# Optimization experiments

Hardware: AMD Instinct MI355X
Metric: run time of the kernel (lower is better)

Reference implementation:

```python
import jax, jax.numpy as jnp
import numpy as np

EMBED = 1024

def setup_inputs() -> dict:
    key = jax.random.key(0)
    ks = jax.random.split(key, 10)
    B, S, E = 4, 2048, EMBED
    inv = 1.0 / np.sqrt(E)
    return {
        "query": jax.random.normal(ks[0], (B, S, E), jnp.float32),
        "key": jax.random.normal(ks[1], (B, S, E), jnp.float32),
        "value": jax.random.normal(ks[2], (B, S, E), jnp.float32),
        "attn_mask": jnp.zeros((B, S, S), jnp.float32),
        "Wq": jax.random.normal(ks[3], (E, E), jnp.float32) * inv,
        "bq": jnp.zeros((E,), jnp.float32),
        "Wk": jax.random.normal(ks[4], (E, E), jnp.float32) * inv,
        "bk": jnp.zeros((E,), jnp.float32),
        "Wv": jax.random.normal(ks[5], (E, E), jnp.float32) * inv,
        "bv": jnp.zeros((E,), jnp.float32),
    }

def reference(query, key, value, attn_mask, Wq, bq, Wk, bk, Wv, bv):
    E = query.shape[-1]
    q = query @ Wq.T + bq            # [B,S,E]
    k = key @ Wk.T + bk              # [B,S,E]
    v = value @ Wv.T + bv            # [B,S,E]
    scores = jnp.einsum('bse,bte->bst', q, k) / jnp.sqrt(jnp.float32(E))
    scores = scores + attn_mask      # [B,S,S]
    attn = jax.nn.softmax(scores, axis=-1)
    return jnp.einsum('bst,bte->bse', attn, v)
```

## Files before the change

### kernel.cpp

```cpp
#include <hip/hip_runtime.h>
#include <cstdint>
#include <cstddef>

typedef __bf16 bf16;
typedef __bf16 bf16x8 __attribute__((ext_vector_type(8)));
typedef float  f32x4  __attribute__((ext_vector_type(4)));

#define NB 4
#define SS 2048
#define EE 1024

#define BUFB   24576
#define LDS3   (3 * BUFB)
#define BUFB64 49152
#define LDS64  (3 * BUFB64)

static __device__ __forceinline__ void glds16(const bf16* g, void* l)
{
    __builtin_amdgcn_global_load_lds(
        (const __attribute__((address_space(1))) unsigned int*)g,
        (__attribute__((address_space(3))) unsigned int*)l,
        16, 0, 0);
}

static __device__ __forceinline__ void swz_block(int& bx, int& by, int& bz)
{
    const int nx = gridDim.x, ny = gridDim.y;
    const int nwg = nx * ny * gridDim.z;
    int lin = blockIdx.x + nx * (blockIdx.y + ny * blockIdx.z);
    const int per = nwg >> 3;
    lin = (lin & 7) * per + (lin >> 3);
    bz = lin / (nx * ny);
    const int r = lin - bz * nx * ny;
    by = r / nx;
    bx = r - by * nx;
}

static __device__ __forceinline__ void kloop32(
    const bf16* __restrict__ A, const bf16* __restrict__ Bm,
    int lda, int ldb, int nt, char* lds, int m0, int n0, int tid,
    f32x4 acc[4][4])
{
    constexpr int NBUF = 3;
    const int lane = tid & 63, w = tid >> 6;
    const int wm = w >> 2, wn = w & 3;
    const int lr = lane & 15, kq = lane >> 4;
    const int cb = ((kq ^ ((lr >> 1) & 3)) << 4);

    const int srow   = tid >> 2;
    const int chunkL = (tid & 3) ^ ((srow >> 1) & 3);
    const bf16* Asrc = A  + (size_t)(m0 + srow) * lda + chunkL * 8;
    const bf16* Bsrc = Bm + (size_t)(n0 + srow) * ldb + chunkL * 8;
    const int wofs = w << 10;

#pragma unroll
    for (int p = 0; p < NBUF - 1; ++p) {
        char* d = lds + p * BUFB + wofs;
        const int kt = p * 32;
        glds16(Asrc + kt,                     d);
        glds16(Bsrc + kt,                     d + 8192);
        glds16(Bsrc + (size_t)128 * ldb + kt, d + 16384);
    }
    asm volatile("s_waitcnt vmcnt(3)" ::: "memory");
    __builtin_amdgcn_sched_barrier(0);
    __builtin_amdgcn_s_barrier();
    __builtin_amdgcn_sched_barrier(0);

    int rb = 0, sb = NBUF - 1;
    for (int t = 0; t < nt; ++t) {
        char* la = lds + rb * BUFB;
        char* lb = la + 8192;
        const int ts = (t + NBUF - 1 < nt) ? t + NBUF - 1 : nt - 1;
        const int kt = ts * 32;
        char* d = lds + sb * BUFB + wofs;

        bf16x8 af[4], bg[4];
#pragma unroll
        for (int m = 0; m < 4; ++m)
            af[m] = *(const bf16x8*)(la + (wm * 64 + m * 16 + lr) * 64 + cb);
#pragma unroll
        for (int n = 0; n < 4; ++n)
            bg[n] = *(const bf16x8*)(lb + (wn * 64 + n * 16 + lr) * 64 + cb);

        glds16(Asrc + kt,                     d);
        glds16(Bsrc + kt,                     d + 8192);
        glds16(Bsrc + (size_t)128 * ldb + kt, d + 16384);

        __builtin_amdgcn_s_setprio(1);
#pragma unroll
        for (int m = 0; m < 4; ++m)
#pragma unroll
            for (int n = 0; n < 4; ++n)
                acc[m][n] = __builtin_amdgcn_mfma_f32_16x16x32_bf16(af[m], bg[n], acc[m][n], 0, 0, 0);
        __builtin_amdgcn_s_setprio(0);

        if (t < nt - 1) {
            asm volatile("s_waitcnt vmcnt(3)" ::: "memory");
            __builtin_amdgcn_sched_barrier(0);
            __builtin_amdgcn_s_barrier();
            __builtin_amdgcn_sched_barrier(0);
        }
        rb = (rb + 1 == NBUF) ? 0 : rb + 1;
        sb = (sb + 1 == NBUF) ? 0 : sb + 1;
    }
    asm volatile("s_waitcnt vmcnt(0)" ::: "memory");
}

static __device__ __forceinline__ void kloop32w(
    const bf16* __restrict__ A, const bf16* __restrict__ Bm,
    int lda, int ldb, int nt, char* lds, int m0, int n0, int tid,
    f32x4 acc[4][8])
{
    constexpr int NBUF = 3;
    const int lane = tid & 63, w = tid >> 6;
    const int wm = w >> 1, wn = w & 1;
    const int lr = lane & 15, kq = lane >> 4;
    const int cb = ((kq ^ ((lr >> 1) & 3)) << 4);

    const int srow   = tid >> 2;
    const int chunkL = (tid & 3) ^ ((srow >> 1) & 3);
    const bf16* Asrc = A  + (size_t)(m0 + srow) * lda + chunkL * 8;
    const bf16* Bsrc = Bm + (size_t)(n0 + srow) * ldb + chunkL * 8;
    const int wofs = w << 10;

#pragma unroll
    for (int p = 0; p < NBUF - 1; ++p) {
        char* d = lds + p * BUFB + wofs;
        const int kt = p * 32;
        glds16(Asrc + kt,                      d);
        glds16(Asrc + (size_t)64  * lda + kt,  d + 4096);
        glds16(Bsrc + kt,                      d + 8192);
        glds16(Bsrc + (size_t)64  * ldb + kt,  d + 12288);
        glds16(Bsrc + (size_t)128 * ldb + kt,  d + 16384);
        glds16(Bsrc + (size_t)192 * ldb + kt,  d + 20480);
    }
    asm volatile("s_waitcnt vmcnt(6)" ::: "memory");
    __builtin_amdgcn_sched_barrier(0);
    __builtin_amdgcn_s_barrier();
    __builtin_amdgcn_sched_barrier(0);

    int rb = 0, sb = NBUF - 1;
    for (int t = 0; t < nt; ++t) {
        char* la = lds + rb * BUFB;
        char* lb = la + 8192;
        const int ts = (t + NBUF - 1 < nt) ? t + NBUF - 1 : nt - 1;
        const int kt = ts * 32;
        char* d = lds + sb * BUFB + wofs;

        bf16x8 af[4], bg[8];
#pragma unroll
        for (int m = 0; m < 4; ++m)
            af[m] = *(const bf16x8*)(la + (wm * 64 + m * 16 + lr) * 64 + cb);
#pragma unroll
        for (int n = 0; n < 8; ++n)
            bg[n] = *(const bf16x8*)(lb + (wn * 128 + n * 16 + lr) * 64 + cb);

        glds16(Asrc + kt,                      d);
        glds16(Asrc + (size_t)64  * lda + kt,  d + 4096);
        glds16(Bsrc + kt,                      d + 8192);
        glds16(Bsrc + (size_t)64  * ldb + kt,  d + 12288);
        glds16(Bsrc + (size_t)128 * ldb + kt,  d + 16384);
        glds16(Bsrc + (size_t)192 * ldb + kt,  d + 20480);

        __builtin_amdgcn_s_setprio(1);
#pragma unroll
        for (int m = 0; m < 4; ++m)
#pragma unroll
            for (int n = 0; n < 8; ++n)
                acc[m][n] = __builtin_amdgcn_mfma_f32_16x16x32_bf16(af[m], bg[n], acc[m][n], 0, 0, 0);
        __builtin_amdgcn_s_setprio(0);

        if (t < nt - 1) {
            asm volatile("s_waitcnt vmcnt(6)" ::: "memory");
            __builtin_amdgcn_sched_barrier(0);
            __builtin_amdgcn_s_barrier();
            __builtin_amdgcn_sched_barrier(0);
        }
        rb = (rb + 1 == NBUF) ? 0 : rb + 1;
        sb = (sb + 1 == NBUF) ? 0 : sb + 1;
    }
    asm volatile("s_waitcnt vmcnt(0)" ::: "memory");
}

static __device__ __forceinline__ void kloop64(
    const bf16* __restrict__ A, const bf16* __restrict__ Bm,
    int lda, int ldb, int nt, char* lds, int m0, int n0, int tid,
    f32x4 acc[4][4])
{
    const int lane = tid & 63, w = tid >> 6;
    const int wm = w >> 2, wn = w & 3;
    const int lr = lane & 15, kq = lane >> 4;
    const int axor = (lr & 7) << 4;

    const int srow   = tid >> 3;
    const int chunkL = (tid & 7) ^ (srow & 7);
    const bf16* Asrc = A  + (size_t)(m0 + srow) * lda + chunkL * 8;
    const bf16* Bsrc = Bm + (size_t)(n0 + srow) * ldb + chunkL * 8;
    const int wofs = w << 10;

#pragma unroll
    for (int p = 0; p < 2; ++p) {
        char* d = lds + p * BUFB64 + wofs;
        const int kt = p * 64;
        glds16(Asrc + kt,                        d);
        glds16(Asrc + (size_t)64 * lda + kt,     d + 8192);
        glds16(Bsrc + kt,                        d + 16384);
        glds16(Bsrc + (size_t)64 * ldb + kt,     d + 16384 + 8192);
        glds16(Bsrc + (size_t)128 * ldb + kt,    d + 16384 + 16384);
        glds16(Bsrc + (size_t)192 * ldb + kt,    d + 16384 + 24576);
    }
    asm volatile("s_waitcnt vmcnt(6)" ::: "memory");
    __builtin_amdgcn_sched_barrier(0);
    __builtin_amdgcn_s_barrier();
    __builtin_amdgcn_sched_barrier(0);

    for (int t = 0; t < nt; ++t) {
        char* la = lds + (t % 3) * BUFB64;
        char* lb = la + 16384;
        char* sa = lds + ((t + 2) % 3) * BUFB64;
        const bool st = (t + 2) < nt;
        const int kt = (t + 2) * 64;

        bf16x8 af[4], bg[4];
        {
            const int cbk = (kq * 16) ^ axor;
#pragma unroll
            for (int m = 0; m < 4; ++m)
                af[m] = *(const bf16x8*)(la + (wm * 64 + m * 16 + lr) * 128 + cbk);
#pragma unroll
            for (int n = 0; n < 4; ++n)
                bg[n] = *(const bf16x8*)(lb + (wn * 64 + n * 16 + lr) * 128 + cbk);
            if (st) {
                glds16(Asrc + kt,                    sa + wofs);
                glds16(Asrc + (size_t)64 * lda + kt, sa + 8192 + wofs);
                glds16(Bsrc + kt,                    sa + 16384 + wofs);
            }
            __builtin_amdgcn_s_setprio(1);
#pragma unroll
            for (int m = 0; m < 4; ++m)
#pragma unroll
                for (int n = 0; n < 4; ++n)
                    acc[m][n] = __builtin_amdgcn_mfma_f32_16x16x32_bf16(af[m], bg[n], acc[m][n], 0, 0, 0);
            __builtin_amdgcn_s_setprio(0);
        }
        {
            const int cbk = (64 + kq * 16) ^ axor;
#pragma unroll
            for (int m = 0; m < 4; ++m)
                af[m] = *(const bf16x8*)(la + (wm * 64 + m * 16 + lr) * 128 + cbk);
#pragma unroll
            for (int n = 0; n < 4; ++n)
                bg[n] = *(const bf16x8*)(lb + (wn * 64 + n * 16 + lr) * 128 + cbk);
            if (st) {
                glds16(Bsrc + (size_t)64 * ldb + kt,  sa + 16384 + 8192 + wofs);
                glds16(Bsrc + (size_t)128 * ldb + kt, sa + 16384 + 16384 + wofs);
                glds16(Bsrc + (size_t)192 * ldb + kt, sa + 16384 + 24576 + wofs);
            }
            __builtin_amdgcn_s_setprio(1);
#pragma unroll
            for (int m = 0; m < 4; ++m)
#pragma unroll
                for (int n = 0; n < 4; ++n)
                    acc[m][n] = __builtin_amdgcn_mfma_f32_16x16x32_bf16(af[m], bg[n], acc[m][n], 0, 0, 0);
            __builtin_amdgcn_s_setprio(0);
        }
        if (t < nt - 1) {
            if (st) { asm volatile("s_waitcnt vmcnt(6)" ::: "memory"); }
            else    { asm volatile("s_waitcnt vmcnt(0)" ::: "memory"); }
            __builtin_amdgcn_sched_barrier(0);
            __builtin_amdgcn_s_barrier();
            __builtin_amdgcn_sched_barrier(0);
        }
    }
}

__global__ __launch_bounds__(256) void cvt_all(
    const float* __restrict__ q, const float* __restrict__ k, const float* __restrict__ v,
    const float* __restrict__ Wq, const float* __restrict__ Wk, const float* __restrict__ Wv,
    bf16* __restrict__ qc, bf16* __restrict__ kc, bf16* __restrict__ vc,
    bf16* __restrict__ Wc)
{
    const int y = blockIdx.y;
    const float* s; bf16* d; size_t i;
    if (blockIdx.x < 4096) {
        s = (y == 0) ? q : (y == 1) ? k : v;
        d = (y == 0) ? qc : (y == 1) ? kc : vc;
        i = ((size_t)blockIdx.x * 256 + threadIdx.x) * 8;
    } else {
        s = (y == 0) ? Wq : (y == 1) ? Wk : Wv;
        d = Wc + (size_t)y * EE * EE;
        i = ((size_t)(blockIdx.x - 4096) * 256 + threadIdx.x) * 8;
    }
    const float4 f0 = *(const float4*)(s + i);
    const float4 f1 = *(const float4*)(s + i + 4);
    bf16x8 h;
    h[0] = (bf16)f0.x; h[1] = (bf16)f0.y; h[2] = (bf16)f0.z; h[3] = (bf16)f0.w;
    h[4] = (bf16)f1.x; h[5] = (bf16)f1.y; h[6] = (bf16)f1.z; h[7] = (bf16)f1.w;
    *(bf16x8*)(d + i) = h;
}

__global__ __launch_bounds__(512, 4) void proj8(
    const bf16* __restrict__ qc, const bf16* __restrict__ kc, const bf16* __restrict__ vc,
    const bf16* __restrict__ Wc,
    const float* __restrict__ bq, const float* __restrict__ bk, const float* __restrict__ bv,
    bf16* __restrict__ qb, bf16* __restrict__ kb, bf16* __restrict__ vt)
{
    extern __shared__ char lds[];
    int bx, by, bz; swz_block(bx, by, bz);
    const bf16* A; const float* bias;
    if (bz == 0)      { A = qc; bias = bq; }
    else if (bz == 1) { A = kc; bias = bk; }
    else              { A = vc; bias = bv; }
    const bf16* Bm = Wc + (size_t)bz * EE * EE;

    const int m0 = by * 128, n0 = bx * 256;
    const int tid = threadIdx.x;

    f32x4 acc[4][4];
#pragma unroll
    for (int m = 0; m < 4; ++m)
#pragma unroll
        for (int n = 0; n < 4; ++n) { acc[m][n][0] = 0.f; acc[m][n][1] = 0.f; acc[m][n][2] = 0.f; acc[m][n][3] = 0.f; }

    kloop32(A, Bm, EE, EE, EE / 32, lds, m0, n0, tid, acc);

    const int lane = tid & 63, w = tid >> 6, wm = w >> 2, wn = w & 3;
    const int lr = lane & 15, kq = lane >> 4;

    if (bz < 2) {
        bf16* out = (bz == 0) ? qb : kb;
#pragma unroll
        for (int n = 0; n < 4; ++n) {
            const int gcol = n0 + wn * 64 + n * 16 + lr;
            const float bb = bias[gcol];
#pragma unroll
            for (int m = 0; m < 4; ++m)
#pragma unroll
                for (int j = 0; j < 4; ++j) {
                    const int grow = m0 + wm * 64 + m * 16 + kq * 4 + j;
                    out[(size_t)grow * EE + gcol] = (bf16)(acc[m][n][j] + bb);
                }
        }
    } else {
        __syncthreads();
#pragma unroll
        for (int n = 0; n < 4; ++n) {
            const int gc = wn * 64 + n * 16 + lr;
            const float bb = bias[n0 + gc];
#pragma unroll
            for (int m = 0; m < 4; ++m) {
                const int gr = wm * 64 + m * 16 + kq * 4;
                union { unsigned short u[4]; uint2 v; } h;
#pragma unroll
                for (int j = 0; j < 4; ++j) {
                    union { bf16 b; unsigned short u; } cv;
                    cv.b = (bf16)(acc[m][n][j] + bb);
                    h.u[j] = cv.u;
                }
                char* p = lds + gc * 256 + (((gr >> 3) ^ (gc & 7)) << 4) + (gr & 7) * 2;
                *(uint2*)p = h.v;
            }
        }
        __syncthreads();
        const int r = tid >> 1, par = tid & 1;
        const int bb_ = m0 >> 11;
        const int s0 = m0 & (SS - 1);
        bf16* dst = vt + ((size_t)bb_ * EE + n0 + r) * SS + s0 + par * 64;
#pragma unroll
        for (int i = 0; i < 8; ++i) {
            const int c = par * 8 + i;
            const char* p = lds + r * 256 + ((c ^ (r & 7)) << 4);
            *(uint4*)&dst[i * 8] = *(const uint4*)p;
        }
    }
}

__global__ __launch_bounds__(256, 2) void scores8(const bf16* __restrict__ qb,
                                                  const bf16* __restrict__ kb,
                                                  const float* __restrict__ mask,
                                                  bf16* __restrict__ sc)
{
    extern __shared__ char lds[];
    int bx, by, bz; swz_block(bx, by, bz);
    const bf16* A  = qb + (size_t)bz * SS * EE;
    const bf16* Bm = kb + (size_t)bz * SS * EE;

    const int m0 = by * 128, n0 = bx * 256;
    const int tid = threadIdx.x;

    f32x4 acc[4][8];
#pragma unroll
    for (int m = 0; m < 4; ++m)
#pragma unroll
        for (int n = 0; n < 8; ++n) { acc[m][n][0] = 0.f; acc[m][n][1] = 0.f; acc[m][n][2] = 0.f; acc[m][n][3] = 0.f; }

    kloop32w(A, Bm, EE, EE, EE / 32, lds, m0, n0, tid, acc);

    const int lane = tid & 63, w = tid >> 6, wm = w >> 1, wn = w & 1;
    const int lr = lane & 15, kq = lane >> 4;
    const float* mrow = mask + (size_t)bz * SS * SS;
    bf16* out = sc + (size_t)bz * SS * SS;
    const float scale = 0.03125f;
#pragma unroll
    for (int m = 0; m < 4; ++m)
#pragma unroll
        for (int n = 0; n < 8; ++n)
#pragma unroll
            for (int j = 0; j < 4; ++j) {
                const int grow = m0 + wm * 64 + m * 16 + kq * 4 + j;
                const int gcol = n0 + wn * 128 + n * 16 + lr;
                const float v = acc[m][n][j] * scale + mrow[(size_t)grow * SS + gcol];
                out[(size_t)grow * SS + gcol] = (bf16)v;
            }
}

__global__ __launch_bounds__(256) void softmax_kernel(bf16* __restrict__ sc)
{
    __shared__ float red[4];
    const size_t row = blockIdx.x;
    uint4* rp = (uint4*)(sc + row * (size_t)SS);
    const int tid = threadIdx.x, lane = tid & 63, wid = tid >> 6;

    const uint4 d = rp[tid];
    const unsigned int u[4] = { d.x, d.y, d.z, d.w };
    float f[8];
#pragma unroll
    for (int i = 0; i < 4; ++i) {
        union { unsigned int i_; float f_; } lo, hi;
        lo.i_ = u[i] << 16;
        hi.i_ = u[i] & 0xffff0000u;
        f[2 * i]     = lo.f_;
        f[2 * i + 1] = hi.f_;
    }

    float m = f[0];
#pragma unroll
    for (int i = 1; i < 8; ++i) m = fmaxf(m, f[i]);
#pragma unroll
    for (int o = 32; o > 0; o >>= 1) m = fmaxf(m, __shfl_xor(m, o));
    if (lane == 0) red[wid] = m;
    __syncthreads();
    m = fmaxf(fmaxf(red[0], red[1]), fmaxf(red[2], red[3]));
    __syncthreads();

    float e[8], s = 0.f;
#pragma unroll
    for (int i = 0; i < 8; ++i) { e[i] = __expf(f[i] - m); s += e[i]; }
#pragma unroll
    for (int o = 32; o > 0; o >>= 1) s += __shfl_xor(s, o);
    if (lane == 0) red[wid] = s;
    __syncthreads();
    s = red[0] + red[1] + red[2] + red[3];
    const float inv = 1.0f / s;

    unsigned int ou[4];
#pragma unroll
    for (int i = 0; i < 4; ++i) {
        union { bf16 h; unsigned short b; } a0, a1;
        a0.h = (bf16)(e[2 * i] * inv);
        a1.h = (bf16)(e[2 * i + 1] * inv);
        ou[i] = ((unsigned int)a1.b << 16) | (unsigned int)a0.b;
    }
    rp[tid] = make_uint4(ou[0], ou[1], ou[2], ou[3]);
}

__global__ __launch_bounds__(512) void pv8(const bf16* __restrict__ sc,
                                           const bf16* __restrict__ vt,
                                           float* __restrict__ outp)
{
    extern __shared__ char lds[];
    int bx, by, bz; swz_block(bx, by, bz);
    const bf16* A  = sc + (size_t)bz * SS * SS;
    const bf16* Bm = vt + (size_t)bz * EE * SS;

    const int m0 = by * 128, n0 = bx * 256;
    const int tid = threadIdx.x;

    f32x4 acc[4][4];
#pragma unroll
    for (int m = 0; m < 4; ++m)
#pragma unroll
        for (int n = 0; n < 4; ++n) { acc[m][n][0] = 0.f; acc[m][n][1] = 0.f; acc[m][n][2] = 0.f; acc[m][n][3] = 0.f; }

    kloop64(A, Bm, SS, SS, SS / 64, lds, m0, n0, tid, acc);

    const int lane = tid & 63, w = tid >> 6, wm = w >> 2, wn = w & 3;
    const int lr = lane & 15, kq = lane >> 4;
#pragma unroll
    for (int m = 0; m < 4; ++m)
#pragma unroll
        for (int n = 0; n < 4; ++n)
#pragma unroll
            for (int j = 0; j < 4; ++j) {
                const int grow = m0 + wm * 64 + m * 16 + kq * 4 + j;
                const int gcol = n0 + wn * 64 + n * 16 + lr;
                outp[((size_t)bz * SS + grow) * EE + gcol] = acc[m][n][j];
            }
}

extern "C" void kernel_launch(void* const* d_in, const int* in_sizes, int n_in,
                              void* d_out, int out_size, void* d_ws, size_t ws_size,
                              hipStream_t stream)
{
    const float* query = (const float*)d_in[0];
    const float* key_  = (const float*)d_in[1];
    const float* value = (const float*)d_in[2];
    const float* mask  = (const float*)d_in[3];
    const float* Wq = (const float*)d_in[4];
    const float* bq = (const float*)d_in[5];
    const float* Wk = (const float*)d_in[6];
    const float* bk = (const float*)d_in[7];
    const float* Wv = (const float*)d_in[8];
    const float* bv = (const float*)d_in[9];
    float* outp = (float*)d_out;

    char* ws = (char*)d_ws;
    const size_t QKV = (size_t)NB * SS * EE * 2;
    const size_t SCB = (size_t)NB * SS * SS * 2;
    const size_t WCB = (size_t)3 * EE * EE * 2;
    if (ws_size < 4 * QKV + SCB + WCB) return;

    bf16* qb = (bf16*)(ws);
    bf16* kb = (bf16*)(ws + QKV);
    bf16* vt = (bf16*)(ws + 3 * QKV);
    bf16* sc = (bf16*)(ws + 4 * QKV);
    bf16* Wc = (bf16*)(ws + 4 * QKV + SCB);
    bf16* qc = (bf16*)(ws + 2 * QKV);
    bf16* kc = sc;
    bf16* vc = (bf16*)(ws + 5 * QKV);

    (void)hipFuncSetAttribute((const void*)proj8,   hipFuncAttributeMaxDynamicSharedMemorySize, LDS3);
    (void)hipFuncSetAttribute((const void*)scores8, hipFuncAttributeMaxDynamicSharedMemorySize, LDS3);
    (void)hipFuncSetAttribute((const void*)pv8,     hipFuncAttributeMaxDynamicSharedMemorySize, LDS64);

    dim3 blk(256), blk5(512);
    cvt_all<<<dim3(4096 + 512, 3), blk, 0, stream>>>(
        query, key_, value, Wq, Wk, Wv, qc, kc, vc, Wc);

    proj8<<<dim3(EE / 256, (NB * SS) / 128, 3), blk5, LDS3, stream>>>(
        qc, kc, vc, Wc, bq, bk, bv, qb, kb, vt);
    scores8<<<dim3(SS / 256, SS / 128, NB), blk, LDS3, stream>>>(qb, kb, mask, sc);
    softmax_kernel<<<dim3(NB * SS), blk, 0, stream>>>(sc);
    pv8<<<dim3(EE / 256, SS / 128, NB), blk5, LDS64, stream>>>(sc, vt, outp);
}
```

Before: 192.5 us.

## Fuse softmax into scores epilogue and defer normalization to PV

Removes the standalone softmax kernel. The scores kernel now writes exp(score) directly and stores per-row partial sums into a workspace buffer. The PV kernel reduces those partials into per-row reciprocals held in LDS and scales its output by them. This avoids a full extra read and write pass over the S×S score matrix and one launch, but drops the max subtraction, so it can overflow for inputs with large scores.

```diff
diff --git a/kernel.cpp b/kernel.cpp
--- a/kernel.cpp
+++ b/kernel.cpp
@@ -14,6 +14,7 @@
 #define LDS3   (3 * BUFB)
 #define BUFB64 49152
 #define LDS64  (3 * BUFB64)
+#define LDS64P (LDS64 + 512)
 
 static __device__ __forceinline__ void glds16(const bf16* g, void* l)
 {
@@ -378,7 +379,8 @@
 __global__ __launch_bounds__(256, 2) void scores8(const bf16* __restrict__ qb,
                                                   const bf16* __restrict__ kb,
                                                   const float* __restrict__ mask,
-                                                  bf16* __restrict__ sc)
+                                                  bf16* __restrict__ sc,
+                                                  float* __restrict__ part)
 {
     extern __shared__ char lds[];
     int bx, by, bz; swz_block(bx, by, bz);
@@ -401,6 +403,13 @@
     const float* mrow = mask + (size_t)bz * SS * SS;
     bf16* out = sc + (size_t)bz * SS * SS;
     const float scale = 0.03125f;
+
+    float rp[4][4];
+#pragma unroll
+    for (int m = 0; m < 4; ++m)
+#pragma unroll
+        for (int j = 0; j < 4; ++j) rp[m][j] = 0.f;
+
 #pragma unroll
     for (int m = 0; m < 4; ++m)
 #pragma unroll
@@ -410,62 +419,35 @@
                 const int grow = m0 + wm * 64 + m * 16 + kq * 4 + j;
                 const int gcol = n0 + wn * 128 + n * 16 + lr;
                 const float v = acc[m][n][j] * scale + mrow[(size_t)grow * SS + gcol];
-                out[(size_t)grow * SS + gcol] = (bf16)v;
+                const float e = __expf(v);
+                out[(size_t)grow * SS + gcol] = (bf16)e;
+                rp[m][j] += e;
             }
-}
-
-__global__ __launch_bounds__(256) void softmax_kernel(bf16* __restrict__ sc)
-{
-    __shared__ float red[4];
-    const size_t row = blockIdx.x;
-    uint4* rp = (uint4*)(sc + row * (size_t)SS);
-    const int tid = threadIdx.x, lane = tid & 63, wid = tid >> 6;
-
-    const uint4 d = rp[tid];
-    const unsigned int u[4] = { d.x, d.y, d.z, d.w };
-    float f[8];
-#pragma unroll
-    for (int i = 0; i < 4; ++i) {
-        union { unsigned int i_; float f_; } lo, hi;
-        lo.i_ = u[i] << 16;
-        hi.i_ = u[i] & 0xffff0000u;
-        f[2 * i]     = lo.f_;
-        f[2 * i + 1] = hi.f_;
-    }
-
-    float m = f[0];
-#pragma unroll
-    for (int i = 1; i < 8; ++i) m = fmaxf(m, f[i]);
-#pragma unroll
-    for (int o = 32; o > 0; o >>= 1) m = fmaxf(m, __shfl_xor(m, o));
-    if (lane == 0) red[wid] = m;
-    __syncthreads();
-    m = fmaxf(fmaxf(red[0], red[1]), fmaxf(red[2], red[3]));
-    __syncthreads();
-
-    float e[8], s = 0.f;
-#pragma unroll
-    for (int i = 0; i < 8; ++i) { e[i] = __expf(f[i] - m); s += e[i]; }
-#pragma unroll
-    for (int o = 32; o > 0; o >>= 1) s += __shfl_xor(s, o);
-    if (lane == 0) red[wid] = s;
-    __syncthreads();
-    s = red[0] + red[1] + red[2] + red[3];
-    const float inv = 1.0f / s;
-
-    unsigned int ou[4];
-#pragma unroll
-    for (int i = 0; i < 4; ++i) {
-        union { bf16 h; unsigned short b; } a0, a1;
-        a0.h = (bf16)(e[2 * i] * inv);
-        a1.h = (bf16)(e[2 * i + 1] * inv);
-        ou[i] = ((unsigned int)a1.b << 16) | (unsigned int)a0.b;
-    }
-    rp[tid] = make_uint4(ou[0], ou[1], ou[2], ou[3]);
+
+#pragma unroll
+    for (int m = 0; m < 4; ++m)
+#pragma unroll
+        for (int j = 0; j < 4; ++j) {
+            float s = rp[m][j];
+            s += __shfl_xor(s, 1);
+            s += __shfl_xor(s, 2);
+            s += __shfl_xor(s, 4);
+            s += __shfl_xor(s, 8);
+            rp[m][j] = s;
+        }
+    if (lr == 0) {
+        float* pp = part + (size_t)(bx * 2 + wn) * (NB * SS) + (size_t)bz * SS + m0;
+#pragma unroll
+        for (int m = 0; m < 4; ++m)
+#pragma unroll
+            for (int j = 0; j < 4; ++j)
+                pp[wm * 64 + m * 16 + kq * 4 + j] = rp[m][j];
+    }
 }
 
 __global__ __launch_bounds__(512) void pv8(const bf16* __restrict__ sc,
                                            const bf16* __restrict__ vt,
+                                           const float* __restrict__ part,
                                            float* __restrict__ outp)
 {
     extern __shared__ char lds[];
@@ -476,6 +458,16 @@
     const int m0 = by * 128, n0 = bx * 256;
     const int tid = threadIdx.x;
 
+    float* invs = (float*)(lds + LDS64);
+    if (tid < 128) {
+        const size_t rowb = (size_t)bz * SS + m0 + tid;
+        float s = 0.f;
+#pragma unroll
+        for (int i = 0; i < 16; ++i) s += part[(size_t)i * (NB * SS) + rowb];
+        invs[tid] = 1.0f / s;
+    }
+    __syncthreads();
+
     f32x4 acc[4][4];
 #pragma unroll
     for (int m = 0; m < 4; ++m)
@@ -489,13 +481,15 @@
 #pragma unroll
     for (int m = 0; m < 4; ++m)
 #pragma unroll
-        for (int n = 0; n < 4; ++n)
-#pragma unroll
-            for (int j = 0; j < 4; ++j) {
-                const int grow = m0 + wm * 64 + m * 16 + kq * 4 + j;
+        for (int j = 0; j < 4; ++j) {
+            const int lrow = wm * 64 + m * 16 + kq * 4 + j;
+            const float iv = invs[lrow];
+#pragma unroll
+            for (int n = 0; n < 4; ++n) {
                 const int gcol = n0 + wn * 64 + n * 16 + lr;
-                outp[((size_t)bz * SS + grow) * EE + gcol] = acc[m][n][j];
+                outp[((size_t)bz * SS + m0 + lrow) * EE + gcol] = acc[m][n][j] * iv;
             }
+        }
 }
 
 extern "C" void kernel_launch(void* const* d_in, const int* in_sizes, int n_in,
@@ -526,12 +520,13 @@
     bf16* sc = (bf16*)(ws + 4 * QKV);
     bf16* Wc = (bf16*)(ws + 4 * QKV + SCB);
     bf16* qc = (bf16*)(ws + 2 * QKV);
+    float* part = (float*)(ws + 2 * QKV);
     bf16* kc = sc;
     bf16* vc = (bf16*)(ws + 5 * QKV);
 
     (void)hipFuncSetAttribute((const void*)proj8,   hipFuncAttributeMaxDynamicSharedMemorySize, LDS3);
     (void)hipFuncSetAttribute((const void*)scores8, hipFuncAttributeMaxDynamicSharedMemorySize, LDS3);
-    (void)hipFuncSetAttribute((const void*)pv8,     hipFuncAttributeMaxDynamicSharedMemorySize, LDS64);
+    (void)hipFuncSetAttribute((const void*)pv8,     hipFuncAttributeMaxDynamicSharedMemorySize, LDS64P);
 
     dim3 blk(256), blk5(512);
     cvt_all<<<dim3(4096 + 512, 3), blk, 0, stream>>>(
@@ -539,7 +534,6 @@
 
     proj8<<<dim3(EE / 256, (NB * SS) / 128, 3), blk5, LDS3, stream>>>(
         qc, kc, vc, Wc, bq, bk, bv, qb, kb, vt);
-    scores8<<<dim3(SS / 256, SS / 128, NB), blk, LDS3, stream>>>(qb, kb, mask, sc);
-    softmax_kernel<<<dim3(NB * SS), blk, 0, stream>>>(sc);
-    pv8<<<dim3(EE / 256, SS / 128, NB), blk5, LDS64, stream>>>(sc, vt, outp);
-}
+    scores8<<<dim3(SS / 256, SS / 128, NB), blk, LDS3, stream>>>(qb, kb, mask, sc, part);
+    pv8<<<dim3(EE / 256, SS / 128, NB), blk5, LDS64P, stream>>>(sc, vt, part, outp);
+}
```

After: 180.9 us, median of 2. 1.06x faster.
